# Optimization experiments

Measured on AMD Instinct MI355X. Metric: run time of the kernel, lower is better.

Reference implementation:

```python
import jax, jax.numpy as jnp
import numpy as np

N_OPENIE = 100000
N_ENTITY = 100000
E = 150000
D_IN = 512
D_OUT = 512
H = 8
DH = D_OUT // H
NEG_SLOPE = 0.2


def setup_inputs() -> dict:
    key = jax.random.key(0)
    ks = jax.random.split(key, 16)
    def rn(k, shape, scale=0.05):
        return jax.random.normal(k, shape, dtype=jnp.float32) * scale
    return {
        "x_openie": jax.random.normal(ks[0], (N_OPENIE, D_IN), dtype=jnp.float32),
        "x_entity": jax.random.normal(ks[1], (N_ENTITY, D_IN), dtype=jnp.float32),
        "edge_e2o": jax.random.randint(ks[2], (2, E), 0, N_OPENIE, dtype=jnp.int32),
        "edge_o2o": jax.random.randint(ks[3], (2, E), 0, N_OPENIE, dtype=jnp.int32),
        "proj_o_w": rn(ks[4], (D_IN, D_OUT)),
        "proj_o_b": jnp.zeros((D_OUT,), jnp.float32),
        "proj_e_w": rn(ks[5], (D_IN, D_OUT)),
        "proj_e_b": jnp.zeros((D_OUT,), jnp.float32),
        "att_src_e2o": rn(ks[6], (H, DH)),
        "att_dst_e2o": rn(ks[7], (H, DH)),
        "att_src_o2o": rn(ks[8], (H, DH)),
        "att_dst_o2o": rn(ks[9], (H, DH)),
        "k_lin_w": rn(ks[10], (D_OUT, D_OUT)),
        "k_lin_b": jnp.zeros((D_OUT,), jnp.float32),
        "q_sem": rn(ks[11], (D_OUT,)),
        "lin_w": rn(ks[12], (D_OUT, 2)),
        "lin_b": jnp.zeros((2,), jnp.float32),
    }


def _edge_type_conv(h_src, h_dst, att_src, att_dst, src, dst, n_dst):
    # GAT-style per-edge-type attention (one metapath of HANConv).
    a_src = jnp.einsum('nhd,hd->nh', h_src, att_src)  # [N_src, H]
    a_dst = jnp.einsum('nhd,hd->nh', h_dst, att_dst)  # [N_dst, H]
    alpha = jax.nn.leaky_relu(a_src[src] + a_dst[dst], NEG_SLOPE)  # [E, H]
    amax = jax.ops.segment_max(alpha, dst, num_segments=n_dst)     # [N_dst, H]
    ex = jnp.exp(alpha - amax[dst])
    denom = jax.ops.segment_sum(ex, dst, num_segments=n_dst)
    w = ex / (denom[dst] + 1e-16)                                   # softmax over in-edges
    msg = h_src[src] * w[:, :, None]                                # [E, H, DH]
    out = jax.ops.segment_sum(msg, dst, num_segments=n_dst)        # [N_dst, H, DH]
    return jax.nn.relu(out.reshape(n_dst, H * DH))


def reference(x_openie, x_entity, edge_e2o, edge_o2o, proj_o_w, proj_o_b, proj_e_w,
              proj_e_b, att_src_e2o, att_dst_e2o, att_src_o2o, att_dst_o2o,
              k_lin_w, k_lin_b, q_sem, lin_w, lin_b):
    # Per-node-type projection to heads
    h_o = (x_openie @ proj_o_w + proj_o_b).reshape(-1, H, DH)
    h_e = (x_entity @ proj_e_w + proj_e_b).reshape(-1, H, DH)
    # Two metapaths ending at 'openie'
    out0 = _edge_type_conv(h_e, h_o, att_src_e2o, att_dst_e2o, edge_e2o[0], edge_e2o[1], N_OPENIE)
    out1 = _edge_type_conv(h_o, h_o, att_src_o2o, att_dst_o2o, edge_o2o[0], edge_o2o[1], N_OPENIE)
    # Semantic-level attention across metapaths
    outs = jnp.stack([out0, out1])                         # [M, N, F]
    k = jnp.tanh(outs @ k_lin_w + k_lin_b).mean(axis=1)    # [M, F]
    sem = jax.nn.softmax((k * q_sem).sum(-1))              # [M]
    fused = jnp.einsum('m,mnf->nf', sem, outs)             # [N, F]
    # global mean pool (single graph) -> dropout (eval: identity) -> Linear(F, 2)
    pooled = fused.mean(axis=0, keepdims=True)             # [1, F]
    return pooled @ lin_w + lin_b                          # [1, 2]
```

## Files before the change

kernel.cpp:

```cpp
#include <hip/hip_runtime.h>
#include <math.h>

#define N_NODES 100000
#define N_EDGES 150000
#define D 512
#define H 8
#define NEG_SLOPE 0.2f

typedef __attribute__((ext_vector_type(8))) short bf16x8;
typedef __attribute__((ext_vector_type(4))) float f32x4;

__device__ __forceinline__ float bf2f(unsigned short u) { return __uint_as_float(((unsigned int)u) << 16); }
__device__ __forceinline__ unsigned short f2bf(float f) {
    unsigned int u = __float_as_uint(f);
    unsigned int r = u + 0x7FFFu + ((u >> 16) & 1u);
    return (unsigned short)(r >> 16);
}
__device__ __forceinline__ unsigned int pkbf(float a, float b) {
    unsigned int ua = __float_as_uint(a) + 0x8000u;
    unsigned int ub = __float_as_uint(b) + 0x8000u;
    return (ua >> 16) | (ub & 0xFFFF0000u);
}
__device__ __forceinline__ void gl_lds16(const void* g, void* l) {
    __builtin_amdgcn_global_load_lds((const __attribute__((address_space(1))) void*)g,
                                     (__attribute__((address_space(3))) void*)l, 16, 0, 0);
}

__global__ __launch_bounds__(256) void zero_kernel(float4* __restrict__ p, int n4) {
    int t = blockIdx.x * 256 + threadIdx.x;
    if (t < n4) p[t] = make_float4(0.f, 0.f, 0.f, 0.f);
}

__global__ __launch_bounds__(256)
void transpose_to_bf16(const float* __restrict__ W, unsigned short* __restrict__ Wt) {
    __shared__ float tile[32][33];
    int bx = blockIdx.x, by = blockIdx.y;
    int t = threadIdx.x, tx = t & 31, ty = t >> 5;
    #pragma unroll
    for (int p = 0; p < 4; ++p) {
        int k = by * 32 + ty + p * 8;
        tile[ty + p * 8][tx] = W[(size_t)k * D + bx * 32 + tx];
    }
    __syncthreads();
    #pragma unroll
    for (int p = 0; p < 4; ++p) {
        int n = bx * 32 + ty + p * 8;
        Wt[(size_t)n * D + by * 32 + tx] = f2bf(tile[tx][ty + p * 8]);
    }
}

__global__ __launch_bounds__(256)
void hist_edges(const int* __restrict__ e2o, const int* __restrict__ o2o, int* __restrict__ deg) {
    int i = blockIdx.x * 256 + threadIdx.x;
    if (i < N_EDGES) atomicAdd(&deg[e2o[N_EDGES + i]], 1);
    else if (i < 2 * N_EDGES) atomicAdd(&deg[N_NODES + o2o[N_EDGES + (i - N_EDGES)]], 1);
}

__global__ __launch_bounds__(256)
void scan1(const int* __restrict__ deg, int* __restrict__ rowptr, int* __restrict__ partials, int n) {
    __shared__ int lds[256];
    int t = threadIdx.x, b = blockIdx.x;
    int base = b * 1024 + t * 4;
    int d0 = (base + 0 < n) ? deg[base + 0] : 0;
    int d1 = (base + 1 < n) ? deg[base + 1] : 0;
    int d2 = (base + 2 < n) ? deg[base + 2] : 0;
    int d3 = (base + 3 < n) ? deg[base + 3] : 0;
    int s = d0 + d1 + d2 + d3;
    lds[t] = s;
    __syncthreads();
    for (int off = 1; off < 256; off <<= 1) {
        int v = (t >= off) ? lds[t - off] : 0;
        __syncthreads();
        lds[t] += v;
        __syncthreads();
    }
    int incl = lds[t];
    int eb = incl - s;
    if (base + 0 < n) rowptr[base + 0] = eb;
    if (base + 1 < n) rowptr[base + 1] = eb + d0;
    if (base + 2 < n) rowptr[base + 2] = eb + d0 + d1;
    if (base + 3 < n) rowptr[base + 3] = eb + d0 + d1 + d2;
    if (t == 255) partials[b] = incl;
}

__global__ __launch_bounds__(256)
void scan2(int* __restrict__ partials, int nb) {
    __shared__ int lds[256];
    int t = threadIdx.x;
    lds[t] = (t < nb) ? partials[t] : 0;
    __syncthreads();
    if (t == 0) {
        int acc = 0;
        for (int i = 0; i < nb; ++i) { int v = lds[i]; lds[i] = acc; acc += v; }
    }
    __syncthreads();
    if (t < nb) partials[t] = lds[t];
}

__global__ __launch_bounds__(256)
void scan3(int* __restrict__ rowptr, const int* __restrict__ partials, int* __restrict__ cursor, int n, int total) {
    int t = threadIdx.x, b = blockIdx.x;
    int base = b * 1024 + t * 4;
    int add = partials[b];
    #pragma unroll
    for (int j = 0; j < 4; ++j) {
        if (base + j < n) {
            int v = rowptr[base + j] + add;
            rowptr[base + j] = v;
            cursor[base + j] = v;
        }
    }
    if (b == 0 && t == 0) rowptr[n] = total;
}

__global__ __launch_bounds__(256)
void fill_csr(const int* __restrict__ e2o, const int* __restrict__ o2o,
              int* __restrict__ cursor, int* __restrict__ csr) {
    int i = blockIdx.x * 256 + threadIdx.x;
    if (i < N_EDGES) {
        int d = e2o[N_EDGES + i];
        int p = atomicAdd(&cursor[d], 1);
        csr[p] = e2o[i];
    } else if (i < 2 * N_EDGES) {
        int j = i - N_EDGES;
        int d = o2o[N_EDGES + j];
        int p = atomicAdd(&cursor[N_NODES + d], 1);
        csr[p] = o2o[j];
    }
}

__global__ __launch_bounds__(256)
void gemm_proj(const float* __restrict__ A, const unsigned short* __restrict__ Bt,
               const float* __restrict__ bias, unsigned short* __restrict__ C, int M)
{
    __shared__ __align__(16) float As32[128 * 32];
    __shared__ __align__(16) unsigned short Bs[128 * 32];
    const int tid = threadIdx.x, lane = tid & 63, wave = tid >> 6;
    const int rb = blockIdx.y * 128, cb = blockIdx.x * 128;
    const int wm = (wave >> 1) * 64, wn = (wave & 1) * 64;

    const float* agp[4]; float* alp[4];
    #pragma unroll
    for (int c = 0; c < 4; ++c) {
        int r = c * 32 + wave * 8 + (lane >> 3);
        int rg = rb + r; if (rg > M - 1) rg = M - 1;
        agp[c] = A + (size_t)rg * D + (lane & 7) * 4;
        alp[c] = &As32[(c * 32 + wave * 8) * 32];
    }
    const unsigned short* bgp[2]; unsigned short* blp[2];
    #pragma unroll
    for (int c = 0; c < 2; ++c) {
        int r = c * 64 + wave * 16 + (lane >> 2);
        bgp[c] = Bt + (size_t)(cb + r) * D + (lane & 3) * 8;
        blp[c] = &Bs[(c * 64 + wave * 16) * 32];
    }

    f32x4 acc[4][4];
    #pragma unroll
    for (int i = 0; i < 4; ++i)
        #pragma unroll
        for (int j = 0; j < 4; ++j) acc[i][j] = (f32x4){0.f, 0.f, 0.f, 0.f};

    const int fro = (lane & 15) * 32 + (lane >> 4) * 8;

    for (int k = 0; k < 16; ++k) {
        if (k) __syncthreads();
        #pragma unroll
        for (int c = 0; c < 4; ++c) { gl_lds16(agp[c], alp[c]); agp[c] += 32; }
        #pragma unroll
        for (int c = 0; c < 2; ++c) { gl_lds16(bgp[c], blp[c]); bgp[c] += 32; }
        __syncthreads();
        bf16x8 af[4], bfr[4];
        #pragma unroll
        for (int mi = 0; mi < 4; ++mi) {
            const float* ar = &As32[(wm + mi * 16 + (lane & 15)) * 32 + (lane >> 4) * 8];
            float4 u0 = *(const float4*)ar;
            float4 u1 = *(const float4*)(ar + 4);
            union { bf16x8 v; unsigned int u[4]; } cv;
            cv.u[0] = pkbf(u0.x, u0.y); cv.u[1] = pkbf(u0.z, u0.w);
            cv.u[2] = pkbf(u1.x, u1.y); cv.u[3] = pkbf(u1.z, u1.w);
            af[mi] = cv.v;
        }
        #pragma unroll
        for (int ni = 0; ni < 4; ++ni) bfr[ni] = *(const bf16x8*)&Bs[(wn + ni * 16) * 32 + fro];
        #pragma unroll
        for (int mi = 0; mi < 4; ++mi)
            #pragma unroll
            for (int ni = 0; ni < 4; ++ni)
                acc[mi][ni] = __builtin_amdgcn_mfma_f32_16x16x32_bf16(af[mi], bfr[ni], acc[mi][ni], 0, 0, 0);
    }

    float bb[4];
    #pragma unroll
    for (int ni = 0; ni < 4; ++ni) bb[ni] = bias[cb + wn + ni * 16 + (lane & 15)];
    #pragma unroll
    for (int mi = 0; mi < 4; ++mi) {
        int rg0 = rb + wm + mi * 16 + (lane >> 4) * 4;
        #pragma unroll
        for (int r = 0; r < 4; ++r) {
            int rg = rg0 + r;
            if (rg < M) {
                size_t base = (size_t)rg * D + cb + wn + (lane & 15);
                #pragma unroll
                for (int ni = 0; ni < 4; ++ni)
                    C[base + ni * 16] = f2bf(acc[mi][ni][r] + bb[ni]);
            }
        }
    }
}

__global__ __launch_bounds__(256)
void gemm_tanh(const unsigned short* __restrict__ A, const unsigned short* __restrict__ Bt,
               const float* __restrict__ bias, float* __restrict__ ksum, int M)
{
    __shared__ __align__(16) unsigned short As[128 * 32];
    __shared__ __align__(16) unsigned short Bs[128 * 32];
    const int tid = threadIdx.x, lane = tid & 63, wave = tid >> 6;
    const int rb = blockIdx.y * 128, cb = blockIdx.x * 128;
    const int wm = (wave >> 1) * 64, wn = (wave & 1) * 64;

    const unsigned short* agp[2]; unsigned short* alp[2];
    const unsigned short* bgp[2]; unsigned short* blp[2];
    #pragma unroll
    for (int c = 0; c < 2; ++c) {
        int r = c * 64 + wave * 16 + (lane >> 2);
        int rg = rb + r; if (rg > M - 1) rg = M - 1;
        agp[c] = A + (size_t)rg * D + (lane & 3) * 8;
        alp[c] = &As[(c * 64 + wave * 16) * 32];
        bgp[c] = Bt + (size_t)(cb + r) * D + (lane & 3) * 8;
        blp[c] = &Bs[(c * 64 + wave * 16) * 32];
    }

    f32x4 acc[4][4];
    #pragma unroll
    for (int i = 0; i < 4; ++i)
        #pragma unroll
        for (int j = 0; j < 4; ++j) acc[i][j] = (f32x4){0.f, 0.f, 0.f, 0.f};

    const int fro = (lane & 15) * 32 + (lane >> 4) * 8;

    for (int k = 0; k < 16; ++k) {
        if (k) __syncthreads();
        #pragma unroll
        for (int c = 0; c < 2; ++c) {
            gl_lds16(agp[c], alp[c]); agp[c] += 32;
            gl_lds16(bgp[c], blp[c]); bgp[c] += 32;
        }
        __syncthreads();
        bf16x8 af[4], bfr[4];
        #pragma unroll
        for (int mi = 0; mi < 4; ++mi) af[mi] = *(const bf16x8*)&As[(wm + mi * 16) * 32 + fro];
        #pragma unroll
        for (int ni = 0; ni < 4; ++ni) bfr[ni] = *(const bf16x8*)&Bs[(wn + ni * 16) * 32 + fro];
        #pragma unroll
        for (int mi = 0; mi < 4; ++mi)
            #pragma unroll
            for (int ni = 0; ni < 4; ++ni)
                acc[mi][ni] = __builtin_amdgcn_mfma_f32_16x16x32_bf16(af[mi], bfr[ni], acc[mi][ni], 0, 0, 0);
    }

    float bb[4];
    #pragma unroll
    for (int ni = 0; ni < 4; ++ni) bb[ni] = bias[cb + wn + ni * 16 + (lane & 15)];
    float cs[4] = {0.f, 0.f, 0.f, 0.f};
    #pragma unroll
    for (int mi = 0; mi < 4; ++mi) {
        int rg0 = rb + wm + mi * 16 + (lane >> 4) * 4;
        #pragma unroll
        for (int r = 0; r < 4; ++r) {
            int rg = rg0 + r;
            if (rg < M) {
                #pragma unroll
                for (int ni = 0; ni < 4; ++ni)
                    cs[ni] += tanhf(acc[mi][ni][r] + bb[ni]);
            }
        }
    }
    __syncthreads();
    float* red = (float*)As;
    if (tid < 128) red[tid] = 0.f;
    __syncthreads();
    #pragma unroll
    for (int ni = 0; ni < 4; ++ni) atomicAdd(&red[wn + ni * 16 + (lane & 15)], cs[ni]);
    __syncthreads();
    if (tid < 128) atomicAdd(&ksum[cb + tid], red[tid]);
}

__global__ __launch_bounds__(256)
void compute_a3(const unsigned short* __restrict__ h, const float* __restrict__ att0,
                const float* __restrict__ att1, const float* __restrict__ att2,
                float* __restrict__ a0, float* __restrict__ a1, float* __restrict__ a2,
                int natt)
{
    int t = blockIdx.x * 256 + threadIdx.x;
    if (t >= N_NODES * H) return;
    int n = t >> 3, hh = t & 7;
    const uint4* hp = (const uint4*)(h + (size_t)n * D + hh * 64);
    const float4* p0 = (const float4*)(att0 + hh * 64);
    const float4* p1 = (const float4*)(att1 + hh * 64);
    const float4* p2 = (const float4*)(att2 + hh * 64);
    float s0 = 0.f, s1 = 0.f, s2 = 0.f;
    #pragma unroll
    for (int q = 0; q < 8; ++q) {
        uint4 u = hp[q];
        float f0 = bf2f((unsigned short)(u.x & 0xFFFF)), f1 = bf2f((unsigned short)(u.x >> 16));
        float f2 = bf2f((unsigned short)(u.y & 0xFFFF)), f3 = bf2f((unsigned short)(u.y >> 16));
        float f4 = bf2f((unsigned short)(u.z & 0xFFFF)), f5 = bf2f((unsigned short)(u.z >> 16));
        float f6 = bf2f((unsigned short)(u.w & 0xFFFF)), f7 = bf2f((unsigned short)(u.w >> 16));
        float4 wa = p0[2 * q], wb = p0[2 * q + 1];
        s0 += f0 * wa.x + f1 * wa.y + f2 * wa.z + f3 * wa.w + f4 * wb.x + f5 * wb.y + f6 * wb.z + f7 * wb.w;
        if (natt > 1) {
            wa = p1[2 * q]; wb = p1[2 * q + 1];
            s1 += f0 * wa.x + f1 * wa.y + f2 * wa.z + f3 * wa.w + f4 * wb.x + f5 * wb.y + f6 * wb.z + f7 * wb.w;
        }
        if (natt > 2) {
            wa = p2[2 * q]; wb = p2[2 * q + 1];
            s2 += f0 * wa.x + f1 * wa.y + f2 * wa.z + f3 * wa.w + f4 * wb.x + f5 * wb.y + f6 * wb.z + f7 * wb.w;
        }
    }
    a0[t] = s0;
    if (natt > 1) a1[t] = s1;
    if (natt > 2) a2[t] = s2;
}

__global__ __launch_bounds__(256)
void aggregate(const int* __restrict__ rowptr, const int* __restrict__ csr_src,
               const float* __restrict__ a_src, const float* __restrict__ a_dst,
               const unsigned short* __restrict__ h_src, unsigned short* __restrict__ outbf)
{
    int wid = (blockIdx.x * 256 + threadIdx.x) >> 6;
    int lane = threadIdx.x & 63;
    if (wid >= N_NODES) return;
    int beg = rowptr[wid], end = rowptr[wid + 1];
    int hh = lane & 7;
    float adst = a_dst[wid * H + hh];

    float amax = -1e30f;
    for (int p = beg; p < end; ++p) {
        int s = csr_src[p];
        float al = a_src[s * H + hh] + adst;
        al = (al >= 0.f) ? al : NEG_SLOPE * al;
        amax = fmaxf(amax, al);
    }
    float denom = 0.f;
    for (int p = beg; p < end; ++p) {
        int s = csr_src[p];
        float al = a_src[s * H + hh] + adst;
        al = (al >= 0.f) ? al : NEG_SLOPE * al;
        denom += expf(al - amax);
    }
    float inv = 1.f / (denom + 1e-16f);

    float acc[8] = {0.f, 0.f, 0.f, 0.f, 0.f, 0.f, 0.f, 0.f};
    for (int p = beg; p < end; ++p) {
        int s = csr_src[p];
        float al = a_src[s * H + hh] + adst;
        al = (al >= 0.f) ? al : NEG_SLOPE * al;
        float w = expf(al - amax) * inv;
        const unsigned short* hp = h_src + (size_t)s * D;
        #pragma unroll
        for (int h2 = 0; h2 < 8; ++h2) {
            float wh = __shfl(w, h2);
            acc[h2] += bf2f(hp[h2 * 64 + lane]) * wh;
        }
    }
    size_t base = (size_t)wid * D;
    #pragma unroll
    for (int h2 = 0; h2 < 8; ++h2)
        outbf[base + h2 * 64 + lane] = f2bf(fmaxf(acc[h2], 0.f));
}

__global__ __launch_bounds__(256)
void colsum_bf16(const unsigned short* __restrict__ ob, float* __restrict__ colsum)
{
    __shared__ float red[512];
    int t = threadIdx.x;
    int r0 = blockIdx.x * 128;
    int c8 = t & 63;
    float s[8] = {0.f, 0.f, 0.f, 0.f, 0.f, 0.f, 0.f, 0.f};
    for (int it = 0; it < 32; ++it) {
        int row = r0 + it * 4 + (t >> 6);
        if (row < N_NODES) {
            uint4 v = *((const uint4*)(ob + (size_t)row * D) + c8);
            s[0] += bf2f((unsigned short)(v.x & 0xFFFF)); s[1] += bf2f((unsigned short)(v.x >> 16));
            s[2] += bf2f((unsigned short)(v.y & 0xFFFF)); s[3] += bf2f((unsigned short)(v.y >> 16));
            s[4] += bf2f((unsigned short)(v.z & 0xFFFF)); s[5] += bf2f((unsigned short)(v.z >> 16));
            s[6] += bf2f((unsigned short)(v.w & 0xFFFF)); s[7] += bf2f((unsigned short)(v.w >> 16));
        }
    }
    red[t] = 0.f; red[t + 256] = 0.f;
    __syncthreads();
    #pragma unroll
    for (int j = 0; j < 8; ++j) atomicAdd(&red[c8 * 8 + j], s[j]);
    __syncthreads();
    atomicAdd(&colsum[t], red[t]);
    atomicAdd(&colsum[t + 256], red[t + 256]);
}

__global__ __launch_bounds__(256)
void finalize(const float* __restrict__ ksum, const float* __restrict__ colsum,
              const float* __restrict__ q_sem, const float* __restrict__ lin_w,
              const float* __restrict__ lin_b, float* __restrict__ dout)
{
    __shared__ float red[256];
    __shared__ float semsh[2];
    int t = threadIdx.x;
    const float invN = 1.0f / (float)N_NODES;
    float p0 = ksum[t] * q_sem[t] + ksum[t + 256] * q_sem[t + 256];
    float p1 = ksum[512 + t] * q_sem[t] + ksum[512 + t + 256] * q_sem[t + 256];

    red[t] = p0; __syncthreads();
    for (int s = 128; s > 0; s >>= 1) { if (t < s) red[t] += red[t + s]; __syncthreads(); }
    float S0 = red[0]; __syncthreads();
    red[t] = p1; __syncthreads();
    for (int s = 128; s > 0; s >>= 1) { if (t < s) red[t] += red[t + s]; __syncthreads(); }
    float S1 = red[0]; __syncthreads();

    if (t == 0) {
        float a0 = S0 * invN, a1 = S1 * invN;
        float mx = fmaxf(a0, a1);
        float e0 = expf(a0 - mx), e1 = expf(a1 - mx);
        semsh[0] = e0 / (e0 + e1);
        semsh[1] = e1 / (e0 + e1);
    }
    __syncthreads();
    float sem0 = semsh[0], sem1 = semsh[1];

    float o0 = 0.f, o1 = 0.f;
    #pragma unroll
    for (int q = 0; q < 2; ++q) {
        int f = t + q * 256;
        float pooled = (sem0 * colsum[f] + sem1 * colsum[512 + f]) * invN;
        o0 += pooled * lin_w[f * 2 + 0];
        o1 += pooled * lin_w[f * 2 + 1];
    }
    red[t] = o0; __syncthreads();
    for (int s = 128; s > 0; s >>= 1) { if (t < s) red[t] += red[t + s]; __syncthreads(); }
    if (t == 0) dout[0] = red[0] + lin_b[0];
    __syncthreads();
    red[t] = o1; __syncthreads();
    for (int s = 128; s > 0; s >>= 1) { if (t < s) red[t] += red[t + s]; __syncthreads(); }
    if (t == 0) dout[1] = red[0] + lin_b[1];
}

extern "C" void kernel_launch(void* const* d_in, const int* in_sizes, int n_in,
                              void* d_out, int out_size, void* d_ws, size_t ws_size,
                              hipStream_t stream)
{
    const float* x_o    = (const float*)d_in[0];
    const float* x_e    = (const float*)d_in[1];
    const int*   e2o    = (const int*)d_in[2];
    const int*   o2o    = (const int*)d_in[3];
    const float* pow_   = (const float*)d_in[4];
    const float* pob    = (const float*)d_in[5];
    const float* pew    = (const float*)d_in[6];
    const float* peb    = (const float*)d_in[7];
    const float* as_e2o = (const float*)d_in[8];
    const float* ad_e2o = (const float*)d_in[9];
    const float* as_o2o = (const float*)d_in[10];
    const float* ad_o2o = (const float*)d_in[11];
    const float* klw    = (const float*)d_in[12];
    const float* klb    = (const float*)d_in[13];
    const float* qsem   = (const float*)d_in[14];
    const float* linw   = (const float*)d_in[15];
    const float* linb   = (const float*)d_in[16];

    char* ws = (char*)d_ws;
    size_t off = 0;
    auto alloc = [&](size_t bytes) { void* p = ws + off; off += (bytes + 255) & ~(size_t)255; return p; };

    unsigned short* h_o   = (unsigned short*)alloc((size_t)N_NODES * D * 2);
    unsigned short* h_e   = (unsigned short*)alloc((size_t)N_NODES * D * 2);
    unsigned short* outbf = (unsigned short*)alloc((size_t)N_NODES * D * 2);
    unsigned short* wt_po = (unsigned short*)alloc((size_t)D * D * 2);
    unsigned short* wt_pe = (unsigned short*)alloc((size_t)D * D * 2);
    unsigned short* wt_kl = (unsigned short*)alloc((size_t)D * D * 2);
    float* aS0 = (float*)alloc((size_t)N_NODES * H * 4);
    float* aD0 = (float*)alloc((size_t)N_NODES * H * 4);
    float* aS1 = (float*)alloc((size_t)N_NODES * H * 4);
    float* aD1 = (float*)alloc((size_t)N_NODES * H * 4);
    float* colsum = (float*)alloc(2048 * 4);
    float* ksum   = colsum + 1024;
    int* deg     = (int*)alloc(2 * N_NODES * 4);
    int* cursor  = (int*)alloc(2 * N_NODES * 4);
    int* rowptr  = (int*)alloc((2 * N_NODES + 1) * 4);
    int* partials= (int*)alloc(256 * 4);
    int* csr     = (int*)alloc(2 * N_EDGES * 4);

    const int NSC = 2 * N_NODES;
    const int NB1 = (NSC + 1023) / 1024;
    const int EH  = (2 * N_EDGES + 255) / 256;

    zero_kernel<<<2, 256, 0, stream>>>((float4*)colsum, 512);
    zero_kernel<<<(NSC / 4 + 255) / 256, 256, 0, stream>>>((float4*)deg, NSC / 4);

    hist_edges<<<EH, 256, 0, stream>>>(e2o, o2o, deg);
    scan1<<<NB1, 256, 0, stream>>>(deg, rowptr, partials, NSC);
    scan2<<<1, 256, 0, stream>>>(partials, NB1);
    scan3<<<NB1, 256, 0, stream>>>(rowptr, partials, cursor, NSC, 2 * N_EDGES);
    fill_csr<<<EH, 256, 0, stream>>>(e2o, o2o, cursor, csr);

    dim3 tg(16, 16);
    transpose_to_bf16<<<tg, 256, 0, stream>>>(pow_, wt_po);
    transpose_to_bf16<<<tg, 256, 0, stream>>>(pew, wt_pe);
    transpose_to_bf16<<<tg, 256, 0, stream>>>(klw, wt_kl);

    dim3 gg(D / 128, (N_NODES + 127) / 128);
    gemm_proj<<<gg, 256, 0, stream>>>(x_o, wt_po, pob, h_o, N_NODES);
    gemm_proj<<<gg, 256, 0, stream>>>(x_e, wt_pe, peb, h_e, N_NODES);

    const int nh_blocks = (N_NODES * H + 255) / 256;
    compute_a3<<<nh_blocks, 256, 0, stream>>>(h_o, ad_e2o, as_o2o, ad_o2o, aD0, aS1, aD1, 3);
    compute_a3<<<nh_blocks, 256, 0, stream>>>(h_e, as_e2o, as_e2o, as_e2o, aS0, aS0, aS0, 1);

    const int agg_blocks = (N_NODES * 64 + 255) / 256;
    const int cs_blocks = (N_NODES + 127) / 128;

    aggregate<<<agg_blocks, 256, 0, stream>>>(rowptr, csr, aS0, aD0, h_e, outbf);
    colsum_bf16<<<cs_blocks, 256, 0, stream>>>(outbf, colsum);
    gemm_tanh<<<gg, 256, 0, stream>>>(outbf, wt_kl, klb, ksum, N_NODES);

    aggregate<<<agg_blocks, 256, 0, stream>>>(rowptr + N_NODES, csr, aS1, aD1, h_o, outbf);
    colsum_bf16<<<cs_blocks, 256, 0, stream>>>(outbf, colsum + 512);
    gemm_tanh<<<gg, 256, 0, stream>>>(outbf, wt_kl, klb, ksum + 512, N_NODES);

    finalize<<<1, 256, 0, stream>>>(ksum, colsum, qsem, linw, linb, (float*)d_out);
}
```

Measured before the change: 1.278 ms.

## Batch both metapaths per launch, fuse attention dots into projection GEMM epilogue

Merges paired kernel launches (both projections, both aggregations, both colsums, both tanh GEMMs, the three weight transposes, and two scan stages) into single launches, and replaces the zero kernels with one memset. The attention-logit dot products move into the projection GEMM epilogue via shuffle reductions, which removes the separate compute_a3 passes that re-read h. The fp32 inputs are converted to bf16 in a standalone pass, and the GEMMs now use an MFMA-fragment-ordered LDS layout and a grouped block-to-tile mapping. The extra conversion pass adds memory traffic and the duplicated output buffers need more workspace.

```diff
diff --git a/kernel.cpp b/kernel.cpp
--- a/kernel.cpp
+++ b/kernel.cpp
@@ -6,6 +6,8 @@
 #define D 512
 #define H 8
 #define NEG_SLOPE 0.2f
+#define NBR 782
+#define NBLK (NBR * 4)
 
 typedef __attribute__((ext_vector_type(8))) short bf16x8;
 typedef __attribute__((ext_vector_type(4))) float f32x4;
@@ -25,28 +27,10 @@
     __builtin_amdgcn_global_load_lds((const __attribute__((address_space(1))) void*)g,
                                      (__attribute__((address_space(3))) void*)l, 16, 0, 0);
 }
-
-__global__ __launch_bounds__(256) void zero_kernel(float4* __restrict__ p, int n4) {
-    int t = blockIdx.x * 256 + threadIdx.x;
-    if (t < n4) p[t] = make_float4(0.f, 0.f, 0.f, 0.f);
-}
-
-__global__ __launch_bounds__(256)
-void transpose_to_bf16(const float* __restrict__ W, unsigned short* __restrict__ Wt) {
-    __shared__ float tile[32][33];
-    int bx = blockIdx.x, by = blockIdx.y;
-    int t = threadIdx.x, tx = t & 31, ty = t >> 5;
-    #pragma unroll
-    for (int p = 0; p < 4; ++p) {
-        int k = by * 32 + ty + p * 8;
-        tile[ty + p * 8][tx] = W[(size_t)k * D + bx * 32 + tx];
-    }
-    __syncthreads();
-    #pragma unroll
-    for (int p = 0; p < 4; ++p) {
-        int n = bx * 32 + ty + p * 8;
-        Wt[(size_t)n * D + by * 32 + tx] = f2bf(tile[tx][ty + p * 8]);
-    }
+__device__ __forceinline__ void map_block(int lin, int& rblk, int& cblk) {
+    int g = lin >> 5;
+    if (g < (NBR >> 3)) { rblk = g * 8 + (lin & 7); cblk = (lin >> 3) & 3; }
+    else { int idx = lin - (NBR >> 3) * 32; rblk = (NBR & ~7) + (idx >> 2); cblk = idx & 3; }
 }
 
 __global__ __launch_bounds__(256)
@@ -84,24 +68,20 @@
 }
 
 __global__ __launch_bounds__(256)
-void scan2(int* __restrict__ partials, int nb) {
+void scan23(int* __restrict__ rowptr, const int* __restrict__ partials,
+            int* __restrict__ cursor, int n, int total, int nb) {
     __shared__ int lds[256];
-    int t = threadIdx.x;
+    int t = threadIdx.x, b = blockIdx.x;
     lds[t] = (t < nb) ? partials[t] : 0;
     __syncthreads();
-    if (t == 0) {
-        int acc = 0;
-        for (int i = 0; i < nb; ++i) { int v = lds[i]; lds[i] = acc; acc += v; }
-    }
-    __syncthreads();
-    if (t < nb) partials[t] = lds[t];
-}
-
-__global__ __launch_bounds__(256)
-void scan3(int* __restrict__ rowptr, const int* __restrict__ partials, int* __restrict__ cursor, int n, int total) {
-    int t = threadIdx.x, b = blockIdx.x;
+    for (int off = 1; off < 256; off <<= 1) {
+        int v = (t >= off) ? lds[t - off] : 0;
+        __syncthreads();
+        lds[t] += v;
+        __syncthreads();
+    }
+    int add = (b == 0) ? 0 : lds[b - 1];
     int base = b * 1024 + t * 4;
-    int add = partials[b];
     #pragma unroll
     for (int j = 0; j < 4; ++j) {
         if (base + j < n) {
@@ -130,29 +110,83 @@
 }
 
 __global__ __launch_bounds__(256)
-void gemm_proj(const float* __restrict__ A, const unsigned short* __restrict__ Bt,
-               const float* __restrict__ bias, unsigned short* __restrict__ C, int M)
+void transpose3(const float* __restrict__ W0, const float* __restrict__ W1, const float* __restrict__ W2,
+                unsigned short* __restrict__ T0, unsigned short* __restrict__ T1, unsigned short* __restrict__ T2) {
+    __shared__ float tile[32][33];
+    int z = blockIdx.z;
+    const float* W = (z == 0) ? W0 : (z == 1) ? W1 : W2;
+    unsigned short* T = (z == 0) ? T0 : (z == 1) ? T1 : T2;
+    int bx = blockIdx.x, by = blockIdx.y;
+    int t = threadIdx.x, tx = t & 31, ty = t >> 5;
+    #pragma unroll
+    for (int p = 0; p < 4; ++p) {
+        int k = by * 32 + ty + p * 8;
+        tile[ty + p * 8][tx] = W[(size_t)k * D + bx * 32 + tx];
+    }
+    __syncthreads();
+    #pragma unroll
+    for (int p = 0; p < 4; ++p) {
+        int n = bx * 32 + ty + p * 8;
+        T[(size_t)n * D + by * 32 + tx] = f2bf(tile[tx][ty + p * 8]);
+    }
+}
+
+__global__ __launch_bounds__(256)
+void convert2(const float4* __restrict__ x0, const float4* __restrict__ x1,
+              uint2* __restrict__ y0, uint2* __restrict__ y1) {
+    const int n4 = N_NODES * D / 4;
+    int i = blockIdx.x * 256 + threadIdx.x;
+    const float4* s; uint2* d; int j;
+    if (i < n4) { s = x0; d = y0; j = i; }
+    else { s = x1; d = y1; j = i - n4; }
+    float4 v = s[j];
+    uint2 o; o.x = pkbf(v.x, v.y); o.y = pkbf(v.z, v.w);
+    d[j] = o;
+}
+
+__global__ __launch_bounds__(256)
+void gemm_proj2(const unsigned short* __restrict__ A0, const unsigned short* __restrict__ A1,
+                const unsigned short* __restrict__ Bt0, const unsigned short* __restrict__ Bt1,
+                const float* __restrict__ b0, const float* __restrict__ b1,
+                unsigned short* __restrict__ C0, unsigned short* __restrict__ C1,
+                const float* __restrict__ at00, const float* __restrict__ at01, const float* __restrict__ at02,
+                float* __restrict__ ao00, float* __restrict__ ao01, float* __restrict__ ao02,
+                const float* __restrict__ at10, float* __restrict__ ao10)
 {
-    __shared__ __align__(16) float As32[128 * 32];
-    __shared__ __align__(16) unsigned short Bs[128 * 32];
+    __shared__ __align__(16) unsigned short As[4096];
+    __shared__ __align__(16) unsigned short Bs[4096];
+    const int M = N_NODES;
+    int lin = blockIdx.x;
+    int half = (lin >= NBLK) ? 1 : 0;
+    lin -= half * NBLK;
+    int rblk, cblk; map_block(lin, rblk, cblk);
+    const unsigned short* A  = half ? A1 : A0;
+    const unsigned short* Bt = half ? Bt1 : Bt0;
+    const float* bias        = half ? b1 : b0;
+    unsigned short* C        = half ? C1 : C0;
+    const int natt = half ? 1 : 3;
+    const float* attA = half ? at10 : at00;
+    const float* attB = at01;
+    const float* attC = at02;
+    float* aoA = half ? ao10 : ao00;
+    float* aoB = ao01;
+    float* aoC = ao02;
+
     const int tid = threadIdx.x, lane = tid & 63, wave = tid >> 6;
-    const int rb = blockIdx.y * 128, cb = blockIdx.x * 128;
+    const int rb = rblk * 128, cb = cblk * 128;
     const int wm = (wave >> 1) * 64, wn = (wave & 1) * 64;
 
-    const float* agp[4]; float* alp[4];
-    #pragma unroll
-    for (int c = 0; c < 4; ++c) {
-        int r = c * 32 + wave * 8 + (lane >> 3);
-        int rg = rb + r; if (rg > M - 1) rg = M - 1;
-        agp[c] = A + (size_t)rg * D + (lane & 7) * 4;
-        alp[c] = &As32[(c * 32 + wave * 8) * 32];
-    }
-    const unsigned short* bgp[2]; unsigned short* blp[2];
+    const unsigned short* agp[2]; const unsigned short* bgp[2];
+    unsigned short *ald[2], *bld[2];
     #pragma unroll
     for (int c = 0; c < 2; ++c) {
-        int r = c * 64 + wave * 16 + (lane >> 2);
-        bgp[c] = Bt + (size_t)(cb + r) * D + (lane & 3) * 8;
-        blp[c] = &Bs[(c * 64 + wave * 16) * 32];
+        int s = wave * 2 + c;
+        int rA = rb + s * 16 + (lane & 15); if (rA > M - 1) rA = M - 1;
+        agp[c] = A + (size_t)rA * D + (lane >> 4) * 8;
+        ald[c] = &As[s * 512];
+        int rB = cb + s * 16 + (lane & 15);
+        bgp[c] = Bt + (size_t)rB * D + (lane >> 4) * 8;
+        bld[c] = &Bs[s * 512];
     }
 
     f32x4 acc[4][4];
@@ -160,29 +194,20 @@
     for (int i = 0; i < 4; ++i)
         #pragma unroll
         for (int j = 0; j < 4; ++j) acc[i][j] = (f32x4){0.f, 0.f, 0.f, 0.f};
-
-    const int fro = (lane & 15) * 32 + (lane >> 4) * 8;
 
     for (int k = 0; k < 16; ++k) {
         if (k) __syncthreads();
         #pragma unroll
-        for (int c = 0; c < 4; ++c) { gl_lds16(agp[c], alp[c]); agp[c] += 32; }
-        #pragma unroll
-        for (int c = 0; c < 2; ++c) { gl_lds16(bgp[c], blp[c]); bgp[c] += 32; }
+        for (int c = 0; c < 2; ++c) {
+            gl_lds16(agp[c], ald[c]); agp[c] += 32;
+            gl_lds16(bgp[c], bld[c]); bgp[c] += 32;
+        }
         __syncthreads();
         bf16x8 af[4], bfr[4];
         #pragma unroll
-        for (int mi = 0; mi < 4; ++mi) {
-            const float* ar = &As32[(wm + mi * 16 + (lane & 15)) * 32 + (lane >> 4) * 8];
-            float4 u0 = *(const float4*)ar;
-            float4 u1 = *(const float4*)(ar + 4);
-            union { bf16x8 v; unsigned int u[4]; } cv;
-            cv.u[0] = pkbf(u0.x, u0.y); cv.u[1] = pkbf(u0.z, u0.w);
-            cv.u[2] = pkbf(u1.x, u1.y); cv.u[3] = pkbf(u1.z, u1.w);
-            af[mi] = cv.v;
-        }
-        #pragma unroll
-        for (int ni = 0; ni < 4; ++ni) bfr[ni] = *(const bf16x8*)&Bs[(wn + ni * 16) * 32 + fro];
+        for (int mi = 0; mi < 4; ++mi) af[mi] = *(const bf16x8*)&As[((wave >> 1) * 4 + mi) * 512 + lane * 8];
+        #pragma unroll
+        for (int ni = 0; ni < 4; ++ni) bfr[ni] = *(const bf16x8*)&Bs[((wave & 1) * 4 + ni) * 512 + lane * 8];
         #pragma unroll
         for (int mi = 0; mi < 4; ++mi)
             #pragma unroll
@@ -190,161 +215,78 @@
                 acc[mi][ni] = __builtin_amdgcn_mfma_f32_16x16x32_bf16(af[mi], bfr[ni], acc[mi][ni], 0, 0, 0);
     }
 
-    float bb[4];
-    #pragma unroll
-    for (int ni = 0; ni < 4; ++ni) bb[ni] = bias[cb + wn + ni * 16 + (lane & 15)];
+    float bb[4], av0[4], av1[4], av2[4];
+    const int head = (cb + wn) >> 6;
+    #pragma unroll
+    for (int ni = 0; ni < 4; ++ni) {
+        int ci = ni * 16 + (lane & 15);
+        bb[ni] = bias[cb + wn + ci];
+        av0[ni] = attA[head * 64 + ci];
+        if (natt > 1) { av1[ni] = attB[head * 64 + ci]; av2[ni] = attC[head * 64 + ci]; }
+    }
     #pragma unroll
     for (int mi = 0; mi < 4; ++mi) {
-        int rg0 = rb + wm + mi * 16 + (lane >> 4) * 4;
         #pragma unroll
         for (int r = 0; r < 4; ++r) {
-            int rg = rg0 + r;
-            if (rg < M) {
+            int rg = rb + wm + mi * 16 + (lane >> 4) * 4 + r;
+            bool ok = rg < M;
+            float v[4];
+            #pragma unroll
+            for (int ni = 0; ni < 4; ++ni) v[ni] = acc[mi][ni][r] + bb[ni];
+            if (ok) {
                 size_t base = (size_t)rg * D + cb + wn + (lane & 15);
                 #pragma unroll
-                for (int ni = 0; ni < 4; ++ni)
-                    C[base + ni * 16] = f2bf(acc[mi][ni][r] + bb[ni]);
+                for (int ni = 0; ni < 4; ++ni) C[base + ni * 16] = f2bf(v[ni]);
             }
-        }
-    }
-}
-
-__global__ __launch_bounds__(256)
-void gemm_tanh(const unsigned short* __restrict__ A, const unsigned short* __restrict__ Bt,
-               const float* __restrict__ bias, float* __restrict__ ksum, int M)
+            float s0 = v[0] * av0[0] + v[1] * av0[1] + v[2] * av0[2] + v[3] * av0[3];
+            float s1 = 0.f, s2 = 0.f;
+            if (natt > 1) {
+                s1 = v[0] * av1[0] + v[1] * av1[1] + v[2] * av1[2] + v[3] * av1[3];
+                s2 = v[0] * av2[0] + v[1] * av2[1] + v[2] * av2[2] + v[3] * av2[3];
+            }
+            #pragma unroll
+            for (int m2 = 1; m2 < 16; m2 <<= 1) {
+                s0 += __shfl_xor(s0, m2);
+                if (natt > 1) { s1 += __shfl_xor(s1, m2); s2 += __shfl_xor(s2, m2); }
+            }
+            if (ok && (lane & 15) == 0) {
+                aoA[rg * H + head] = s0;
+                if (natt > 1) { aoB[rg * H + head] = s1; aoC[rg * H + head] = s2; }
+            }
+        }
+    }
+}
+
+__global__ __launch_bounds__(256)
+void aggregate2(const int* __restrict__ rowptr, const int* __restrict__ csr,
+                const float* __restrict__ aS0, const float* __restrict__ aD0, const unsigned short* __restrict__ hE,
+                const float* __restrict__ aS1, const float* __restrict__ aD1, const unsigned short* __restrict__ hO,
+                unsigned short* __restrict__ out0, unsigned short* __restrict__ out1)
 {
-    __shared__ __align__(16) unsigned short As[128 * 32];
-    __shared__ __align__(16) unsigned short Bs[128 * 32];
-    const int tid = threadIdx.x, lane = tid & 63, wave = tid >> 6;
-    const int rb = blockIdx.y * 128, cb = blockIdx.x * 128;
-    const int wm = (wave >> 1) * 64, wn = (wave & 1) * 64;
-
-    const unsigned short* agp[2]; unsigned short* alp[2];
-    const unsigned short* bgp[2]; unsigned short* blp[2];
-    #pragma unroll
-    for (int c = 0; c < 2; ++c) {
-        int r = c * 64 + wave * 16 + (lane >> 2);
-        int rg = rb + r; if (rg > M - 1) rg = M - 1;
-        agp[c] = A + (size_t)rg * D + (lane & 3) * 8;
-        alp[c] = &As[(c * 64 + wave * 16) * 32];
-        bgp[c] = Bt + (size_t)(cb + r) * D + (lane & 3) * 8;
-        blp[c] = &Bs[(c * 64 + wave * 16) * 32];
-    }
-
-    f32x4 acc[4][4];
-    #pragma unroll
-    for (int i = 0; i < 4; ++i)
-        #pragma unroll
-        for (int j = 0; j < 4; ++j) acc[i][j] = (f32x4){0.f, 0.f, 0.f, 0.f};
-
-    const int fro = (lane & 15) * 32 + (lane >> 4) * 8;
-
-    for (int k = 0; k < 16; ++k) {
-        if (k) __syncthreads();
-        #pragma unroll
-        for (int c = 0; c < 2; ++c) {
-            gl_lds16(agp[c], alp[c]); agp[c] += 32;
-            gl_lds16(bgp[c], blp[c]); bgp[c] += 32;
-        }
-        __syncthreads();
-        bf16x8 af[4], bfr[4];
-        #pragma unroll
-        for (int mi = 0; mi < 4; ++mi) af[mi] = *(const bf16x8*)&As[(wm + mi * 16) * 32 + fro];
-        #pragma unroll
-        for (int ni = 0; ni < 4; ++ni) bfr[ni] = *(const bf16x8*)&Bs[(wn + ni * 16) * 32 + fro];
-        #pragma unroll
-        for (int mi = 0; mi < 4; ++mi)
-            #pragma unroll
-            for (int ni = 0; ni < 4; ++ni)
-                acc[mi][ni] = __builtin_amdgcn_mfma_f32_16x16x32_bf16(af[mi], bfr[ni], acc[mi][ni], 0, 0, 0);
-    }
-
-    float bb[4];
-    #pragma unroll
-    for (int ni = 0; ni < 4; ++ni) bb[ni] = bias[cb + wn + ni * 16 + (lane & 15)];
-    float cs[4] = {0.f, 0.f, 0.f, 0.f};
-    #pragma unroll
-    for (int mi = 0; mi < 4; ++mi) {
-        int rg0 = rb + wm + mi * 16 + (lane >> 4) * 4;
-        #pragma unroll
-        for (int r = 0; r < 4; ++r) {
-            int rg = rg0 + r;
-            if (rg < M) {
-                #pragma unroll
-                for (int ni = 0; ni < 4; ++ni)
-                    cs[ni] += tanhf(acc[mi][ni][r] + bb[ni]);
-            }
-        }
-    }
-    __syncthreads();
-    float* red = (float*)As;
-    if (tid < 128) red[tid] = 0.f;
-    __syncthreads();
-    #pragma unroll
-    for (int ni = 0; ni < 4; ++ni) atomicAdd(&red[wn + ni * 16 + (lane & 15)], cs[ni]);
-    __syncthreads();
-    if (tid < 128) atomicAdd(&ksum[cb + tid], red[tid]);
-}
-
-__global__ __launch_bounds__(256)
-void compute_a3(const unsigned short* __restrict__ h, const float* __restrict__ att0,
-                const float* __restrict__ att1, const float* __restrict__ att2,
-                float* __restrict__ a0, float* __restrict__ a1, float* __restrict__ a2,
-                int natt)
-{
-    int t = blockIdx.x * 256 + threadIdx.x;
-    if (t >= N_NODES * H) return;
-    int n = t >> 3, hh = t & 7;
-    const uint4* hp = (const uint4*)(h + (size_t)n * D + hh * 64);
-    const float4* p0 = (const float4*)(att0 + hh * 64);
-    const float4* p1 = (const float4*)(att1 + hh * 64);
-    const float4* p2 = (const float4*)(att2 + hh * 64);
-    float s0 = 0.f, s1 = 0.f, s2 = 0.f;
-    #pragma unroll
-    for (int q = 0; q < 8; ++q) {
-        uint4 u = hp[q];
-        float f0 = bf2f((unsigned short)(u.x & 0xFFFF)), f1 = bf2f((unsigned short)(u.x >> 16));
-        float f2 = bf2f((unsigned short)(u.y & 0xFFFF)), f3 = bf2f((unsigned short)(u.y >> 16));
-        float f4 = bf2f((unsigned short)(u.z & 0xFFFF)), f5 = bf2f((unsigned short)(u.z >> 16));
-        float f6 = bf2f((unsigned short)(u.w & 0xFFFF)), f7 = bf2f((unsigned short)(u.w >> 16));
-        float4 wa = p0[2 * q], wb = p0[2 * q + 1];
-        s0 += f0 * wa.x + f1 * wa.y + f2 * wa.z + f3 * wa.w + f4 * wb.x + f5 * wb.y + f6 * wb.z + f7 * wb.w;
-        if (natt > 1) {
-            wa = p1[2 * q]; wb = p1[2 * q + 1];
-            s1 += f0 * wa.x + f1 * wa.y + f2 * wa.z + f3 * wa.w + f4 * wb.x + f5 * wb.y + f6 * wb.z + f7 * wb.w;
-        }
-        if (natt > 2) {
-            wa = p2[2 * q]; wb = p2[2 * q + 1];
-            s2 += f0 * wa.x + f1 * wa.y + f2 * wa.z + f3 * wa.w + f4 * wb.x + f5 * wb.y + f6 * wb.z + f7 * wb.w;
-        }
-    }
-    a0[t] = s0;
-    if (natt > 1) a1[t] = s1;
-    if (natt > 2) a2[t] = s2;
-}
-
-__global__ __launch_bounds__(256)
-void aggregate(const int* __restrict__ rowptr, const int* __restrict__ csr_src,
-               const float* __restrict__ a_src, const float* __restrict__ a_dst,
-               const unsigned short* __restrict__ h_src, unsigned short* __restrict__ outbf)
-{
-    int wid = (blockIdx.x * 256 + threadIdx.x) >> 6;
+    int gw = (blockIdx.x * 256 + threadIdx.x) >> 6;
     int lane = threadIdx.x & 63;
-    if (wid >= N_NODES) return;
-    int beg = rowptr[wid], end = rowptr[wid + 1];
+    if (gw >= 2 * N_NODES) return;
+    int half = gw >= N_NODES;
+    int node = gw - half * N_NODES;
+    const float* a_src = half ? aS1 : aS0;
+    const float* a_dst = half ? aD1 : aD0;
+    const unsigned short* h = half ? hO : hE;
+    unsigned short* out = half ? out1 : out0;
+
+    int beg = rowptr[gw], end = rowptr[gw + 1];
     int hh = lane & 7;
-    float adst = a_dst[wid * H + hh];
+    float adst = a_dst[node * H + hh];
 
     float amax = -1e30f;
     for (int p = beg; p < end; ++p) {
-        int s = csr_src[p];
+        int s = csr[p];
         float al = a_src[s * H + hh] + adst;
         al = (al >= 0.f) ? al : NEG_SLOPE * al;
         amax = fmaxf(amax, al);
     }
     float denom = 0.f;
     for (int p = beg; p < end; ++p) {
-        int s = csr_src[p];
+        int s = csr[p];
         float al = a_src[s * H + hh] + adst;
         al = (al >= 0.f) ? al : NEG_SLOPE * al;
         denom += expf(al - amax);
@@ -353,29 +295,34 @@
 
     float acc[8] = {0.f, 0.f, 0.f, 0.f, 0.f, 0.f, 0.f, 0.f};
     for (int p = beg; p < end; ++p) {
-        int s = csr_src[p];
+        int s = csr[p];
         float al = a_src[s * H + hh] + adst;
         al = (al >= 0.f) ? al : NEG_SLOPE * al;
         float w = expf(al - amax) * inv;
-        const unsigned short* hp = h_src + (size_t)s * D;
+        const unsigned short* hp = h + (size_t)s * D;
         #pragma unroll
         for (int h2 = 0; h2 < 8; ++h2) {
             float wh = __shfl(w, h2);
             acc[h2] += bf2f(hp[h2 * 64 + lane]) * wh;
         }
     }
-    size_t base = (size_t)wid * D;
+    size_t base = (size_t)node * D;
     #pragma unroll
     for (int h2 = 0; h2 < 8; ++h2)
-        outbf[base + h2 * 64 + lane] = f2bf(fmaxf(acc[h2], 0.f));
-}
-
-__global__ __launch_bounds__(256)
-void colsum_bf16(const unsigned short* __restrict__ ob, float* __restrict__ colsum)
+        out[base + h2 * 64 + lane] = f2bf(fmaxf(acc[h2], 0.f));
+}
+
+__global__ __launch_bounds__(256)
+void colsum2(const unsigned short* __restrict__ ob0, const unsigned short* __restrict__ ob1,
+             float* __restrict__ colsum)
 {
     __shared__ float red[512];
+    int b = blockIdx.x;
+    int half = b >= NBR;
+    const unsigned short* ob = half ? ob1 : ob0;
+    float* cs = colsum + half * 512;
     int t = threadIdx.x;
-    int r0 = blockIdx.x * 128;
+    int r0 = (b - half * NBR) * 128;
     int c8 = t & 63;
     float s[8] = {0.f, 0.f, 0.f, 0.f, 0.f, 0.f, 0.f, 0.f};
     for (int it = 0; it < 32; ++it) {
@@ -393,8 +340,92 @@
     #pragma unroll
     for (int j = 0; j < 8; ++j) atomicAdd(&red[c8 * 8 + j], s[j]);
     __syncthreads();
-    atomicAdd(&colsum[t], red[t]);
-    atomicAdd(&colsum[t + 256], red[t + 256]);
+    atomicAdd(&cs[t & 511], red[t]);
+    atomicAdd(&cs[(t + 256) & 511], red[t + 256]);
+}
+
+__global__ __launch_bounds__(256)
+void gemm_tanh2(const unsigned short* __restrict__ Ah0, const unsigned short* __restrict__ Ah1,
+                const unsigned short* __restrict__ Bt, const float* __restrict__ bias,
+                float* __restrict__ ksum)
+{
+    __shared__ __align__(16) unsigned short As[4096];
+    __shared__ __align__(16) unsigned short Bs[4096];
+    const int M = N_NODES;
+    int lin = blockIdx.x;
+    int half = (lin >= NBLK) ? 1 : 0;
+    lin -= half * NBLK;
+    int rblk, cblk; map_block(lin, rblk, cblk);
+    const unsigned short* A = half ? Ah1 : Ah0;
+    float* ks = ksum + half * 512;
+
+    const int tid = threadIdx.x, lane = tid & 63, wave = tid >> 6;
+    const int rb = rblk * 128, cb = cblk * 128;
+    const int wm = (wave >> 1) * 64, wn = (wave & 1) * 64;
+
+    const unsigned short* agp[2]; const unsigned short* bgp[2];
+    unsigned short *ald[2], *bld[2];
+    #pragma unroll
+    for (int c = 0; c < 2; ++c) {
+        int s = wave * 2 + c;
+        int rA = rb + s * 16 + (lane & 15); if (rA > M - 1) rA = M - 1;
+        agp[c] = A + (size_t)rA * D + (lane >> 4) * 8;
+        ald[c] = &As[s * 512];
+        int rB = cb + s * 16 + (lane & 15);
+        bgp[c] = Bt + (size_t)rB * D + (lane >> 4) * 8;
+        bld[c] = &Bs[s * 512];
+    }
+
+    f32x4 acc[4][4];
+    #pragma unroll
+    for (int i = 0; i < 4; ++i)
+        #pragma unroll
+        for (int j = 0; j < 4; ++j) acc[i][j] = (f32x4){0.f, 0.f, 0.f, 0.f};
+
+    for (int k = 0; k < 16; ++k) {
+        if (k) __syncthreads();
+        #pragma unroll
+        for (int c = 0; c < 2; ++c) {
+            gl_lds16(agp[c], ald[c]); agp[c] += 32;
+            gl_lds16(bgp[c], bld[c]); bgp[c] += 32;
+        }
+        __syncthreads();
+        bf16x8 af[4], bfr[4];
+        #pragma unroll
+        for (int mi = 0; mi < 4; ++mi) af[mi] = *(const bf16x8*)&As[((wave >> 1) * 4 + mi) * 512 + lane * 8];
+        #pragma unroll
+        for (int ni = 0; ni < 4; ++ni) bfr[ni] = *(const bf16x8*)&Bs[((wave & 1) * 4 + ni) * 512 + lane * 8];
+        #pragma unroll
+        for (int mi = 0; mi < 4; ++mi)
+            #pragma unroll
+            for (int ni = 0; ni < 4; ++ni)
+                acc[mi][ni] = __builtin_amdgcn_mfma_f32_16x16x32_bf16(af[mi], bfr[ni], acc[mi][ni], 0, 0, 0);
+    }
+
+    float bb[4];
+    #pragma unroll
+    for (int ni = 0; ni < 4; ++ni) bb[ni] = bias[cb + wn + ni * 16 + (lane & 15)];
+    float cs[4] = {0.f, 0.f, 0.f, 0.f};
+    #pragma unroll
+    for (int mi = 0; mi < 4; ++mi) {
+        #pragma unroll
+        for (int r = 0; r < 4; ++r) {
+            int rg = rb + wm + mi * 16 + (lane >> 4) * 4 + r;
+            if (rg < M) {
+                #pragma unroll
+                for (int ni = 0; ni < 4; ++ni)
+                    cs[ni] += tanhf(acc[mi][ni][r] + bb[ni]);
+            }
+        }
+    }
+    __syncthreads();
+    float* red = (float*)As;
+    if (tid < 128) red[tid] = 0.f;
+    __syncthreads();
+    #pragma unroll
+    for (int ni = 0; ni < 4; ++ni) atomicAdd(&red[wn + ni * 16 + (lane & 15)], cs[ni]);
+    __syncthreads();
+    if (tid < 128) atomicAdd(&ks[cb + tid], red[tid]);
 }
 
 __global__ __launch_bounds__(256)
@@ -469,9 +500,12 @@
     size_t off = 0;
     auto alloc = [&](size_t bytes) { void* p = ws + off; off += (bytes + 255) & ~(size_t)255; return p; };
 
+    unsigned short* xbf_o = (unsigned short*)alloc((size_t)N_NODES * D * 2);
+    unsigned short* xbf_e = (unsigned short*)alloc((size_t)N_NODES * D * 2);
     unsigned short* h_o   = (unsigned short*)alloc((size_t)N_NODES * D * 2);
     unsigned short* h_e   = (unsigned short*)alloc((size_t)N_NODES * D * 2);
-    unsigned short* outbf = (unsigned short*)alloc((size_t)N_NODES * D * 2);
+    unsigned short* obf0  = (unsigned short*)alloc((size_t)N_NODES * D * 2);
+    unsigned short* obf1  = (unsigned short*)alloc((size_t)N_NODES * D * 2);
     unsigned short* wt_po = (unsigned short*)alloc((size_t)D * D * 2);
     unsigned short* wt_pe = (unsigned short*)alloc((size_t)D * D * 2);
     unsigned short* wt_kl = (unsigned short*)alloc((size_t)D * D * 2);
@@ -479,9 +513,10 @@
     float* aD0 = (float*)alloc((size_t)N_NODES * H * 4);
     float* aS1 = (float*)alloc((size_t)N_NODES * H * 4);
     float* aD1 = (float*)alloc((size_t)N_NODES * H * 4);
-    float* colsum = (float*)alloc(2048 * 4);
+    int* misc    = (int*)alloc((2048 + 2 * N_NODES) * 4);
+    float* colsum = (float*)misc;
     float* ksum   = colsum + 1024;
-    int* deg     = (int*)alloc(2 * N_NODES * 4);
+    int* deg      = misc + 2048;
     int* cursor  = (int*)alloc(2 * N_NODES * 4);
     int* rowptr  = (int*)alloc((2 * N_NODES + 1) * 4);
     int* partials= (int*)alloc(256 * 4);
@@ -491,38 +526,26 @@
     const int NB1 = (NSC + 1023) / 1024;
     const int EH  = (2 * N_EDGES + 255) / 256;
 
-    zero_kernel<<<2, 256, 0, stream>>>((float4*)colsum, 512);
-    zero_kernel<<<(NSC / 4 + 255) / 256, 256, 0, stream>>>((float4*)deg, NSC / 4);
+    hipMemsetAsync(misc, 0, (size_t)(2048 + 2 * N_NODES) * 4, stream);
 
     hist_edges<<<EH, 256, 0, stream>>>(e2o, o2o, deg);
     scan1<<<NB1, 256, 0, stream>>>(deg, rowptr, partials, NSC);
-    scan2<<<1, 256, 0, stream>>>(partials, NB1);
-    scan3<<<NB1, 256, 0, stream>>>(rowptr, partials, cursor, NSC, 2 * N_EDGES);
+    scan23<<<NB1, 256, 0, stream>>>(rowptr, partials, cursor, NSC, 2 * N_EDGES, NB1);
     fill_csr<<<EH, 256, 0, stream>>>(e2o, o2o, cursor, csr);
 
-    dim3 tg(16, 16);
-    transpose_to_bf16<<<tg, 256, 0, stream>>>(pow_, wt_po);
-    transpose_to_bf16<<<tg, 256, 0, stream>>>(pew, wt_pe);
-    transpose_to_bf16<<<tg, 256, 0, stream>>>(klw, wt_kl);
-
-    dim3 gg(D / 128, (N_NODES + 127) / 128);
-    gemm_proj<<<gg, 256, 0, stream>>>(x_o, wt_po, pob, h_o, N_NODES);
-    gemm_proj<<<gg, 256, 0, stream>>>(x_e, wt_pe, peb, h_e, N_NODES);
-
-    const int nh_blocks = (N_NODES * H + 255) / 256;
-    compute_a3<<<nh_blocks, 256, 0, stream>>>(h_o, ad_e2o, as_o2o, ad_o2o, aD0, aS1, aD1, 3);
-    compute_a3<<<nh_blocks, 256, 0, stream>>>(h_e, as_e2o, as_e2o, as_e2o, aS0, aS0, aS0, 1);
-
-    const int agg_blocks = (N_NODES * 64 + 255) / 256;
-    const int cs_blocks = (N_NODES + 127) / 128;
-
-    aggregate<<<agg_blocks, 256, 0, stream>>>(rowptr, csr, aS0, aD0, h_e, outbf);
-    colsum_bf16<<<cs_blocks, 256, 0, stream>>>(outbf, colsum);
-    gemm_tanh<<<gg, 256, 0, stream>>>(outbf, wt_kl, klb, ksum, N_NODES);
-
-    aggregate<<<agg_blocks, 256, 0, stream>>>(rowptr + N_NODES, csr, aS1, aD1, h_o, outbf);
-    colsum_bf16<<<cs_blocks, 256, 0, stream>>>(outbf, colsum + 512);
-    gemm_tanh<<<gg, 256, 0, stream>>>(outbf, wt_kl, klb, ksum + 512, N_NODES);
+    transpose3<<<dim3(16, 16, 3), 256, 0, stream>>>(pow_, pew, klw, wt_po, wt_pe, wt_kl);
+    convert2<<<(2 * N_NODES * D / 4) / 256, 256, 0, stream>>>(
+        (const float4*)x_o, (const float4*)x_e, (uint2*)xbf_o, (uint2*)xbf_e);
+
+    gemm_proj2<<<2 * NBLK, 256, 0, stream>>>(
+        xbf_o, xbf_e, wt_po, wt_pe, pob, peb, h_o, h_e,
+        ad_e2o, as_o2o, ad_o2o, aD0, aS1, aD1,
+        as_e2o, aS0);
+
+    aggregate2<<<(2 * N_NODES * 64) / 256, 256, 0, stream>>>(
+        rowptr, csr, aS0, aD0, h_e, aS1, aD1, h_o, obf0, obf1);
+    colsum2<<<2 * NBR, 256, 0, stream>>>(obf0, obf1, colsum);
+    gemm_tanh2<<<2 * NBLK, 256, 0, stream>>>(obf0, obf1, wt_kl, klb, ksum);
 
     finalize<<<1, 256, 0, stream>>>(ksum, colsum, qsem, linw, linb, (float*)d_out);
 }
```

Result: faster. 1.253 ms (-2.0%).
